# Optimization experiments

Hardware: AMD Instinct MI355X
Metric: run time of the kernel (lower is better)

Reference implementation:

```python
import jax, jax.numpy as jnp
import numpy as np

B, L, S = 1, 2048, 2048
D_MODEL, H = 1024, 16
DK = D_MODEL // H  # d_keys = d_values = 64


def sparsemax(z):
    # sparsemax along last axis: proj of z onto the simplex
    K = z.shape[-1]
    z_sorted = jnp.flip(jnp.sort(z, axis=-1), axis=-1)
    cs = jnp.cumsum(z_sorted, axis=-1)
    r = jnp.arange(1, K + 1, dtype=z.dtype)
    support = 1.0 + r * z_sorted > cs
    k = jnp.sum(support, axis=-1, keepdims=True)
    tau = (jnp.take_along_axis(cs, k.astype(jnp.int32) - 1, axis=-1) - 1.0) / k.astype(z.dtype)
    return jnp.maximum(z - tau, 0.0)


def setup_inputs() -> dict:
    key = jax.random.key(0)
    ks = jax.random.split(key, 12)
    sc = 1.0 / np.sqrt(D_MODEL)
    return {
        "queries": jax.random.normal(ks[0], (B, L, D_MODEL), jnp.float32),
        "keys": jax.random.normal(ks[1], (B, S, D_MODEL), jnp.float32),
        "values": jax.random.normal(ks[2], (B, S, D_MODEL), jnp.float32),
        "Wq": jax.random.normal(ks[3], (D_MODEL, H * DK), jnp.float32) * sc,
        "bq": jnp.zeros((H * DK,), jnp.float32),
        "Wk": jax.random.normal(ks[4], (D_MODEL, H * DK), jnp.float32) * sc,
        "bk": jnp.zeros((H * DK,), jnp.float32),
        "Wv": jax.random.normal(ks[5], (H * DK, H * DK), jnp.float32) * sc,
        "bv": jnp.zeros((H * DK,), jnp.float32),
        "Wo": jax.random.normal(ks[6], (H * DK, D_MODEL), jnp.float32) * sc,
        "bo": jnp.zeros((D_MODEL,), jnp.float32),
    }


def reference(queries, keys, values, Wq, bq, Wk, bk, Wv, bv, Wo, bo):
    # projections (note: input `values` is unused, matching the torch source)
    q = (queries @ Wq + bq).reshape(B, L, H, DK)
    k_flat = keys @ Wk + bk                      # [B,S,H*DK]
    k = k_flat.reshape(B, S, H, DK)
    v = (k_flat @ Wv + bv).reshape(B, S, H, DK)  # value_projection(key_projection(keys))
    scale = 1.0 / np.sqrt(DK)
    scores = jnp.einsum('blhe,bshe->bhls', q, k) * scale  # [B,H,L,S]
    A = sparsemax(scores)
    out = jnp.einsum('bhls,bshd->blhd', A, v)             # [B,L,H,DK]
    # mix=True: transpose(2,1) -> [B,H,L,D] then view(B,L,-1)
    out = jnp.swapaxes(out, 1, 2).reshape(B, L, H * DK)
    return out @ Wo + bo
```

## Files before the change

### kernel.cpp

```cpp
#include <hip/hip_runtime.h>
#include <hip/hip_bf16.h>


typedef __attribute__((ext_vector_type(8))) short short8;
typedef __attribute__((ext_vector_type(4))) float floatx4;

#define SRC_BF16 0
#define SRC_F32  1
#define SRC_RT   2
#define CAP 256

__device__ __forceinline__ short f2bf(float f) {
    __hip_bfloat16 h = __float2bfloat16(f);
    return *reinterpret_cast<const short*>(&h);
}
__device__ __forceinline__ unsigned short f2bfu(float f) {
    __hip_bfloat16 h = __float2bfloat16(f);
    return *reinterpret_cast<const unsigned short*>(&h);
}
__device__ __forceinline__ float bf2f(unsigned short u) {
    return __uint_as_float(((unsigned)u) << 16);
}
__device__ __forceinline__ unsigned fmap(float f) {
    unsigned u = __float_as_uint(f);
    return (u & 0x80000000u) ? ~u : (u | 0x80000000u);
}
__device__ __forceinline__ float funmap(unsigned u) {
    return (u & 0x80000000u) ? __uint_as_float(u ^ 0x80000000u) : __uint_as_float(~u);
}

__global__ void detect_k(const short* __restrict__ q, int n, int* __restrict__ flag)
{
    const int tid = threadIdx.x;
    int bad = 0;
    for (int i = tid; i < n; i += 64) {
        float f = bf2f((unsigned short)q[i]);
        if (!(fabsf(f) < 1e10f)) bad = 1;
    }
    unsigned long long m = __ballot(bad != 0);
    if (tid == 0) *flag = (m != 0ULL) ? 1 : 0;
}

__global__ __launch_bounds__(256)
void convert2_k(const void* __restrict__ s0, const void* __restrict__ s1,
                short* __restrict__ d0, short* __restrict__ d1,
                const int* __restrict__ dflag)
{
    const void* s = blockIdx.z ? s1 : s0;
    short* d = blockIdx.z ? d1 : d0;
    const size_t i = ((size_t)blockIdx.x * 256 + threadIdx.x) * 8;
    short8 o;
    if (*dflag) {
        const float4 f0 = ((const float4*)((const float*)s + i))[0];
        const float4 f1 = ((const float4*)((const float*)s + i))[1];
        o[0] = f2bf(f0.x); o[1] = f2bf(f0.y); o[2] = f2bf(f0.z); o[3] = f2bf(f0.w);
        o[4] = f2bf(f1.x); o[5] = f2bf(f1.y); o[6] = f2bf(f1.z); o[7] = f2bf(f1.w);
    } else {
        o = *(const short8*)((const short*)s + i);
    }
    *(short8*)(d + i) = o;
}

struct TP4 {
    const void* s[4];
    short* d[4];
};
__global__ __launch_bounds__(256)
void transpose4_k(TP4 p, int R, int C, const int* __restrict__ dflag)
{
    __shared__ short T[64][72];
    const int tid = threadIdx.x;
    const int bC = blockIdx.x, bR = blockIdx.y;
    const void* src = p.s[blockIdx.z];
    short* dst = p.d[blockIdx.z];
    const bool f32 = (*dflag != 0);

    const int colg = (tid & 7) * 8;
    #pragma unroll
    for (int h = 0; h < 2; ++h) {
        const int row = (tid >> 3) + 32 * h;
        const size_t idx = (size_t)(bR * 64 + row) * (size_t)C + (size_t)(bC * 64 + colg);
        short e[8];
        if (f32) {
            const float4 f0 = ((const float4*)((const float*)src + idx))[0];
            const float4 f1 = ((const float4*)((const float*)src + idx))[1];
            e[0] = f2bf(f0.x); e[1] = f2bf(f0.y); e[2] = f2bf(f0.z); e[3] = f2bf(f0.w);
            e[4] = f2bf(f1.x); e[5] = f2bf(f1.y); e[6] = f2bf(f1.z); e[7] = f2bf(f1.w);
        } else {
            short8 s = *(const short8*)((const short*)src + idx);
            #pragma unroll
            for (int j = 0; j < 8; ++j) e[j] = s[j];
        }
        #pragma unroll
        for (int j = 0; j < 8; ++j) T[colg + j][row] = e[j];
    }
    __syncthreads();
    #pragma unroll
    for (int h = 0; h < 2; ++h) {
        const int orow = (tid >> 3) + 32 * h;
        const int ocolg = (tid & 7) * 8;
        const size_t idx = (size_t)(bC * 64 + orow) * (size_t)R + (size_t)(bR * 64 + ocolg);
        *(short8*)(dst + idx) = *(const short8*)&T[orow][ocolg];
    }
}

struct GJ { const short* A; const short* B; const void* bias; void* C; };

template<int OSRC>
__global__ __launch_bounds__(256)
void gemm64_bt_k(GJ j0, GJ j1, const int* __restrict__ dflag)
{
    __shared__ __align__(16) short As[64][40];
    __shared__ __align__(16) short Bs[64][40];

    const GJ j = blockIdx.z ? j1 : j0;
    const int rtf = *dflag;

    const int tid  = threadIdx.x;
    const int bN   = blockIdx.x, bM = blockIdx.y;
    const int lane = tid & 63, wave = tid >> 6;
    const int wm   = (wave >> 1) * 32;
    const int wn   = (wave & 1) * 32;
    const int quad = lane >> 4, r16 = lane & 15;

    floatx4 acc[2][2];
    #pragma unroll
    for (int i = 0; i < 2; ++i)
        #pragma unroll
        for (int jj = 0; jj < 2; ++jj)
            acc[i][jj] = (floatx4){0.f, 0.f, 0.f, 0.f};

    const int ar = tid >> 2, ac = (tid & 3) * 8;

    for (int k0 = 0; k0 < 1024; k0 += 32) {
        *(short8*)&As[ar][ac] =
            *(const short8*)(j.A + (size_t)(bM * 64 + ar) * 1024 + (size_t)(k0 + ac));
        *(short8*)&Bs[ar][ac] =
            *(const short8*)(j.B + (size_t)(bN * 64 + ar) * 1024 + (size_t)(k0 + ac));
        __syncthreads();

        short8 a0 = *(const short8*)&As[wm + r16][quad * 8];
        short8 a1 = *(const short8*)&As[wm + 16 + r16][quad * 8];
        short8 b0 = *(const short8*)&Bs[wn + r16][quad * 8];
        short8 b1 = *(const short8*)&Bs[wn + 16 + r16][quad * 8];

        acc[0][0] = __builtin_amdgcn_mfma_f32_16x16x32_bf16(a0, b0, acc[0][0], 0, 0, 0);
        acc[0][1] = __builtin_amdgcn_mfma_f32_16x16x32_bf16(a0, b1, acc[0][1], 0, 0, 0);
        acc[1][0] = __builtin_amdgcn_mfma_f32_16x16x32_bf16(a1, b0, acc[1][0], 0, 0, 0);
        acc[1][1] = __builtin_amdgcn_mfma_f32_16x16x32_bf16(a1, b1, acc[1][1], 0, 0, 0);
        __syncthreads();
    }

    const bool of32 = (OSRC == SRC_F32) || (OSRC == SRC_RT && rtf);
    #pragma unroll
    for (int jj = 0; jj < 2; ++jj) {
        const int gc = bN * 64 + wn + jj * 16 + r16;
        const float bb = rtf ? ((const float*)j.bias)[gc]
                             : bf2f(((const unsigned short*)j.bias)[gc]);
        #pragma unroll
        for (int i = 0; i < 2; ++i) {
            #pragma unroll
            for (int rg = 0; rg < 4; ++rg) {
                const int gr = bM * 64 + wm + i * 16 + quad * 4 + rg;
                const float v = acc[i][jj][rg] + bb;
                if (of32)
                    ((float*)j.C)[(size_t)gr * 1024 + gc] = v;
                else
                    ((__hip_bfloat16*)j.C)[(size_t)gr * 1024 + gc] = __float2bfloat16(v);
            }
        }
    }
}

__global__ __launch_bounds__(256)
void attn_fused_k(const short* __restrict__ Qb, const short* __restrict__ Kb,
                  const short* __restrict__ Vb, short* __restrict__ Ob)
{
    __shared__ __align__(16) short sQ[32][72];
    __shared__ __align__(16) short sK[256][72];
    __shared__ unsigned cpk[32][CAP];
    __shared__ unsigned rmax[32];
    __shared__ int cnt[32];

    const int tid  = threadIdx.x;
    const int lane = tid & 63, wave = tid >> 6;
    const int quad = lane >> 4, r16 = lane & 15;
    const int row0 = blockIdx.x * 32;
    const int h    = blockIdx.y;
    const int sp   = (wave >> 1) * 16;
    const int hf   = wave & 1;
    const int myrow = sp + quad * 4;

    if (tid < 32) { rmax[tid] = 0u; cnt[tid] = 0; }
    {
        const int r = tid >> 3, c = (tid & 7) * 8;
        *(short8*)&sQ[r][c] = *(const short8*)(Qb + (size_t)(row0 + r) * 1024 + h * 64 + c);
    }
    __syncthreads();

    const short8 a0 = *(const short8*)&sQ[sp + r16][quad * 8];
    const short8 a1 = *(const short8*)&sQ[sp + r16][32 + quad * 8];

    for (int s0 = 0; s0 < 2048; s0 += 256) {
        #pragma unroll
        for (int i = 0; i < 8; ++i) {
            const int kr = (tid >> 3) + 32 * i, c = (tid & 7) * 8;
            *(short8*)&sK[kr][c] = *(const short8*)(Kb + (size_t)(s0 + kr) * 1024 + h * 64 + c);
        }
        __syncthreads();

        floatx4 acc[8];
        #pragma unroll
        for (int t = 0; t < 8; ++t) {
            const int ct = (hf + 2 * t) * 16;
            const short8 b0 = *(const short8*)&sK[ct + r16][quad * 8];
            const short8 b1 = *(const short8*)&sK[ct + r16][32 + quad * 8];
            floatx4 a = (floatx4){0.f, 0.f, 0.f, 0.f};
            a = __builtin_amdgcn_mfma_f32_16x16x32_bf16(a0, b0, a, 0, 0, 0);
            a = __builtin_amdgcn_mfma_f32_16x16x32_bf16(a1, b1, a, 0, 0, 0);
            #pragma unroll
            for (int rg = 0; rg < 4; ++rg) a[rg] *= 0.125f;
            acc[t] = a;
        }

        #pragma unroll
        for (int rg = 0; rg < 4; ++rg) {
            float m = acc[0][rg];
            #pragma unroll
            for (int t = 1; t < 8; ++t) m = fmaxf(m, acc[t][rg]);
            #pragma unroll
            for (int off = 1; off < 16; off <<= 1)
                m = fmaxf(m, __shfl_xor(m, off, 64));
            if (r16 == 0) atomicMax(&rmax[myrow + rg], fmap(m));
        }
        __syncthreads();

        #pragma unroll
        for (int rg = 0; rg < 4; ++rg) {
            const int row = myrow + rg;
            const float thr = funmap(rmax[row]) - 1.0f;
            #pragma unroll
            for (int t = 0; t < 8; ++t) {
                const float val = acc[t][rg];
                if (val >= thr) {
                    const int p = atomicAdd(&cnt[row], 1);
                    if (p < CAP) {
                        cpk[row][p] = ((unsigned)f2bfu(val) << 16)
                                    | (unsigned)(s0 + (hf + 2 * t) * 16 + r16);
                    }
                }
            }
        }
    }
    __syncthreads();

    const unsigned long long pre = (1ULL << lane) - 1ULL;
    for (int rr = 0; rr < 8; ++rr) {
        const int r = wave * 8 + rr;
        const int n = min(cnt[r], CAP);

        float v[4];
        unsigned short ii[4];
        #pragma unroll
        for (int i = 0; i < 4; ++i) {
            const int ix = lane + i * 64;
            if (ix < n) {
                const unsigned u = cpk[r][ix];
                v[i] = bf2f((unsigned short)(u >> 16));
                ii[i] = (unsigned short)(u & 0xFFFFu);
            } else { v[i] = -3.0e38f; ii[i] = 0; }
        }

        float tau = -3.0e38f, prevc = -1.0f;
        for (int it = 0; it < 24; ++it) {
            float s = 0.f, c = 0.f;
            #pragma unroll
            for (int i = 0; i < 4; ++i)
                if (v[i] > tau) { s += v[i]; c += 1.f; }
            #pragma unroll
            for (int off = 1; off < 64; off <<= 1) {
                s += __shfl_xor(s, off, 64);
                c += __shfl_xor(c, off, 64);
            }
            if (c == prevc) break;
            prevc = c;
            tau = (s - 1.0f) / c;
        }

        int base = 0;
        #pragma unroll
        for (int i = 0; i < 4; ++i) {
            const float p = v[i] - tau;
            const unsigned long long m = __ballot(p > 0.f);
            const int w = base + __popcll(m & pre);
            if (p > 0.f) cpk[r][w] = ((unsigned)f2bfu(p) << 16) | (unsigned)ii[i];
            base += __popcll(m);
        }
        const int msup = base;

        const unsigned short* vb = (const unsigned short*)Vb + (size_t)h * 64 + lane;
        float a0 = 0.f, a1 = 0.f, a2 = 0.f, a3 = 0.f;
        int jj = 0;
        for (; jj + 4 <= msup; jj += 4) {
            const unsigned u0 = cpk[r][jj],     u1 = cpk[r][jj + 1];
            const unsigned u2 = cpk[r][jj + 2], u3 = cpk[r][jj + 3];
            a0 += bf2f((unsigned short)(u0 >> 16)) * bf2f(vb[(size_t)(u0 & 0xFFFFu) * 1024]);
            a1 += bf2f((unsigned short)(u1 >> 16)) * bf2f(vb[(size_t)(u1 & 0xFFFFu) * 1024]);
            a2 += bf2f((unsigned short)(u2 >> 16)) * bf2f(vb[(size_t)(u2 & 0xFFFFu) * 1024]);
            a3 += bf2f((unsigned short)(u3 >> 16)) * bf2f(vb[(size_t)(u3 & 0xFFFFu) * 1024]);
        }
        for (; jj < msup; ++jj) {
            const unsigned u0 = cpk[r][jj];
            a0 += bf2f((unsigned short)(u0 >> 16)) * bf2f(vb[(size_t)(u0 & 0xFFFFu) * 1024]);
        }
        Ob[((size_t)h * 2048 + row0 + r) * 64 + lane] = f2bf(a0 + a1 + a2 + a3);
    }
}

extern "C" void kernel_launch(void* const* d_in, const int* in_sizes, int n_in,
                              void* d_out, int out_size, void* d_ws, size_t ws_size,
                              hipStream_t stream)
{
    (void)in_sizes; (void)n_in; (void)out_size; (void)ws_size;

    const void* queries = d_in[0];
    const void* keys    = d_in[1];
    const void* Wq = d_in[3];
    const void* bq = d_in[4];
    const void* Wk = d_in[5];
    const void* bk = d_in[6];
    const void* Wv = d_in[7];
    const void* bv = d_in[8];
    const void* Wo = d_in[9];
    const void* bo = d_in[10];

    const int L = 2048, DM = 1024;
    const size_t LD = (size_t)L * DM;

    int*   flag = (int*)d_ws;
    short* Qc  = (short*)((char*)d_ws + 256);
    short* Kc  = Qc + LD;
    short* WqT = Kc + LD;
    short* WkT = WqT + (size_t)DM * DM;
    short* WvT = WkT + (size_t)DM * DM;
    short* WoT = WvT + (size_t)DM * DM;
    short* Qb  = WoT + (size_t)DM * DM;
    short* Kb  = Qb + LD;
    short* Vb  = Kb + LD;
    short* Ob  = Vb + LD;

    dim3 blk(256);

    detect_k<<<dim3(1), dim3(64), 0, stream>>>((const short*)queries, 4096, flag);

    convert2_k<<<dim3((unsigned)(LD / 2048), 1, 2), blk, 0, stream>>>(
        queries, keys, Qc, Kc, flag);

    {
        TP4 p;
        p.s[0] = Wq; p.s[1] = Wk; p.s[2] = Wv; p.s[3] = Wo;
        p.d[0] = WqT; p.d[1] = WkT; p.d[2] = WvT; p.d[3] = WoT;
        transpose4_k<<<dim3(DM / 64, DM / 64, 4), blk, 0, stream>>>(p, DM, DM, flag);
    }

    {
        GJ jq{(const short*)Qc, WqT, bq, Qb};
        GJ jk{(const short*)Kc, WkT, bk, Kb};
        gemm64_bt_k<SRC_BF16><<<dim3(DM / 64, L / 64, 2), blk, 0, stream>>>(jq, jk, flag);
    }
    {
        GJ jv{(const short*)Kb, WvT, bv, Vb};
        gemm64_bt_k<SRC_BF16><<<dim3(DM / 64, L / 64, 1), blk, 0, stream>>>(jv, jv, flag);
    }

    attn_fused_k<<<dim3(L / 32, 16), blk, 0, stream>>>(Qb, Kb, Vb, Ob);

    {
        GJ jo{(const short*)Ob, WoT, bo, d_out};
        gemm64_bt_k<SRC_RT><<<dim3(DM / 64, L / 64, 1), blk, 0, stream>>>(jo, jo, flag);
    }
}
```

Measured before the change: 277.3 us.

## Tighten sparsemax candidate threshold with top-2 tracking and aggregate atomics per quad

Each thread now tracks the per-row top-two scores seen so far and uses max(g1-1, (g1+m2-1)/2) as the candidate threshold. This bound is tighter than g1-1, so fewer candidates are pushed to shared memory. Per-element atomicAdd on the row counter is replaced by one ballot-based atomicAdd per 16-lane group. The K tile shrinks to 128 rows and the candidate cap to 128, which cuts LDS use and allows a 4-blocks-per-CU launch bound for higher occupancy. The risk is that rows with more than 128 candidates are silently truncated, and there are twice as many tile iterations and syncs.

Result: faster. 271.7 us (-2.0%).

```diff
diff --git a/kernel.cpp b/kernel.cpp
--- a/kernel.cpp
+++ b/kernel.cpp
@@ -8,7 +8,7 @@
 #define SRC_BF16 0
 #define SRC_F32  1
 #define SRC_RT   2
-#define CAP 256
+#define CAP 128
 
 __device__ __forceinline__ short f2bf(float f) {
     __hip_bfloat16 h = __float2bfloat16(f);
@@ -172,12 +172,12 @@
     }
 }
 
-__global__ __launch_bounds__(256)
+__global__ __launch_bounds__(256, 4)
 void attn_fused_k(const short* __restrict__ Qb, const short* __restrict__ Kb,
                   const short* __restrict__ Vb, short* __restrict__ Ob)
 {
     __shared__ __align__(16) short sQ[32][72];
-    __shared__ __align__(16) short sK[256][72];
+    __shared__ __align__(16) short sK[128][72];
     __shared__ unsigned cpk[32][CAP];
     __shared__ unsigned rmax[32];
     __shared__ int cnt[32];
@@ -198,26 +198,30 @@
     }
     __syncthreads();
 
-    const short8 a0 = *(const short8*)&sQ[sp + r16][quad * 8];
-    const short8 a1 = *(const short8*)&sQ[sp + r16][32 + quad * 8];
-
-    for (int s0 = 0; s0 < 2048; s0 += 256) {
-        #pragma unroll
-        for (int i = 0; i < 8; ++i) {
+    const short8 qa0 = *(const short8*)&sQ[sp + r16][quad * 8];
+    const short8 qa1 = *(const short8*)&sQ[sp + r16][32 + quad * 8];
+
+    float rm1[4], rm2[4];
+    #pragma unroll
+    for (int rg = 0; rg < 4; ++rg) { rm1[rg] = -3.0e38f; rm2[rg] = -3.0e38f; }
+
+    for (int s0 = 0; s0 < 2048; s0 += 128) {
+        #pragma unroll
+        for (int i = 0; i < 4; ++i) {
             const int kr = (tid >> 3) + 32 * i, c = (tid & 7) * 8;
             *(short8*)&sK[kr][c] = *(const short8*)(Kb + (size_t)(s0 + kr) * 1024 + h * 64 + c);
         }
         __syncthreads();
 
-        floatx4 acc[8];
-        #pragma unroll
-        for (int t = 0; t < 8; ++t) {
+        floatx4 acc[4];
+        #pragma unroll
+        for (int t = 0; t < 4; ++t) {
             const int ct = (hf + 2 * t) * 16;
             const short8 b0 = *(const short8*)&sK[ct + r16][quad * 8];
             const short8 b1 = *(const short8*)&sK[ct + r16][32 + quad * 8];
             floatx4 a = (floatx4){0.f, 0.f, 0.f, 0.f};
-            a = __builtin_amdgcn_mfma_f32_16x16x32_bf16(a0, b0, a, 0, 0, 0);
-            a = __builtin_amdgcn_mfma_f32_16x16x32_bf16(a1, b1, a, 0, 0, 0);
+            a = __builtin_amdgcn_mfma_f32_16x16x32_bf16(qa0, b0, a, 0, 0, 0);
+            a = __builtin_amdgcn_mfma_f32_16x16x32_bf16(qa1, b1, a, 0, 0, 0);
             #pragma unroll
             for (int rg = 0; rg < 4; ++rg) a[rg] *= 0.125f;
             acc[t] = a;
@@ -225,29 +229,46 @@
 
         #pragma unroll
         for (int rg = 0; rg < 4; ++rg) {
-            float m = acc[0][rg];
-            #pragma unroll
-            for (int t = 1; t < 8; ++t) m = fmaxf(m, acc[t][rg]);
-            #pragma unroll
-            for (int off = 1; off < 16; off <<= 1)
-                m = fmaxf(m, __shfl_xor(m, off, 64));
-            if (r16 == 0) atomicMax(&rmax[myrow + rg], fmap(m));
+            float m1ab = fmaxf(acc[0][rg], acc[1][rg]);
+            float m2ab = fminf(acc[0][rg], acc[1][rg]);
+            float m1cd = fmaxf(acc[2][rg], acc[3][rg]);
+            float m2cd = fminf(acc[2][rg], acc[3][rg]);
+            float m1 = fmaxf(m1ab, m1cd);
+            float m2 = fmaxf(fminf(m1ab, m1cd), (m1ab >= m1cd) ? m2ab : m2cd);
+            #pragma unroll
+            for (int off = 1; off < 16; off <<= 1) {
+                const float o1 = __shfl_xor(m1, off, 64);
+                const float o2 = __shfl_xor(m2, off, 64);
+                const float n2 = fmaxf(fminf(m1, o1), (m1 >= o1) ? m2 : o2);
+                m1 = fmaxf(m1, o1);
+                m2 = n2;
+            }
+            const float n1 = fmaxf(rm1[rg], m1);
+            rm2[rg] = fmaxf(fminf(rm1[rg], m1), (rm1[rg] >= m1) ? rm2[rg] : m2);
+            rm1[rg] = n1;
+            if (r16 == 0) atomicMax(&rmax[myrow + rg], fmap(m1));
         }
         __syncthreads();
 
         #pragma unroll
         for (int rg = 0; rg < 4; ++rg) {
             const int row = myrow + rg;
-            const float thr = funmap(rmax[row]) - 1.0f;
-            #pragma unroll
-            for (int t = 0; t < 8; ++t) {
+            const float g1 = funmap(rmax[row]);
+            const float thr = fmaxf(g1 - 1.0f, 0.5f * (g1 + rm2[rg]) - 0.5f);
+            #pragma unroll
+            for (int t = 0; t < 4; ++t) {
                 const float val = acc[t][rg];
-                if (val >= thr) {
-                    const int p = atomicAdd(&cnt[row], 1);
-                    if (p < CAP) {
+                const bool keep = (val >= thr);
+                const unsigned long long m = __ballot(keep);
+                const unsigned qm = (unsigned)((m >> (quad * 16)) & 0xFFFFull);
+                int base = 0;
+                if (r16 == 0 && qm) base = atomicAdd(&cnt[row], __popc(qm));
+                base = __shfl(base, quad * 16, 64);
+                if (keep) {
+                    const int p = base + __popc(qm & ((1u << r16) - 1u));
+                    if (p < CAP)
                         cpk[row][p] = ((unsigned)f2bfu(val) << 16)
                                     | (unsigned)(s0 + (hf + 2 * t) * 16 + r16);
-                    }
                 }
             }
         }
@@ -259,10 +280,10 @@
         const int r = wave * 8 + rr;
         const int n = min(cnt[r], CAP);
 
-        float v[4];
-        unsigned short ii[4];
-        #pragma unroll
-        for (int i = 0; i < 4; ++i) {
+        float v[2];
+        unsigned short ii[2];
+        #pragma unroll
+        for (int i = 0; i < 2; ++i) {
             const int ix = lane + i * 64;
             if (ix < n) {
                 const unsigned u = cpk[r][ix];
@@ -275,7 +296,7 @@
         for (int it = 0; it < 24; ++it) {
             float s = 0.f, c = 0.f;
             #pragma unroll
-            for (int i = 0; i < 4; ++i)
+            for (int i = 0; i < 2; ++i)
                 if (v[i] > tau) { s += v[i]; c += 1.f; }
             #pragma unroll
             for (int off = 1; off < 64; off <<= 1) {
@@ -289,7 +310,7 @@
 
         int base = 0;
         #pragma unroll
-        for (int i = 0; i < 4; ++i) {
+        for (int i = 0; i < 2; ++i) {
             const float p = v[i] - tau;
             const unsigned long long m = __ballot(p > 0.f);
             const int w = base + __popcll(m & pre);
@@ -299,21 +320,21 @@
         const int msup = base;
 
         const unsigned short* vb = (const unsigned short*)Vb + (size_t)h * 64 + lane;
-        float a0 = 0.f, a1 = 0.f, a2 = 0.f, a3 = 0.f;
+        float o0 = 0.f, o1 = 0.f, o2 = 0.f, o3 = 0.f;
         int jj = 0;
         for (; jj + 4 <= msup; jj += 4) {
             const unsigned u0 = cpk[r][jj],     u1 = cpk[r][jj + 1];
             const unsigned u2 = cpk[r][jj + 2], u3 = cpk[r][jj + 3];
-            a0 += bf2f((unsigned short)(u0 >> 16)) * bf2f(vb[(size_t)(u0 & 0xFFFFu) * 1024]);
-            a1 += bf2f((unsigned short)(u1 >> 16)) * bf2f(vb[(size_t)(u1 & 0xFFFFu) * 1024]);
-            a2 += bf2f((unsigned short)(u2 >> 16)) * bf2f(vb[(size_t)(u2 & 0xFFFFu) * 1024]);
-            a3 += bf2f((unsigned short)(u3 >> 16)) * bf2f(vb[(size_t)(u3 & 0xFFFFu) * 1024]);
+            o0 += bf2f((unsigned short)(u0 >> 16)) * bf2f(vb[(size_t)(u0 & 0xFFFFu) * 1024]);
+            o1 += bf2f((unsigned short)(u1 >> 16)) * bf2f(vb[(size_t)(u1 & 0xFFFFu) * 1024]);
+            o2 += bf2f((unsigned short)(u2 >> 16)) * bf2f(vb[(size_t)(u2 & 0xFFFFu) * 1024]);
+            o3 += bf2f((unsigned short)(u3 >> 16)) * bf2f(vb[(size_t)(u3 & 0xFFFFu) * 1024]);
         }
         for (; jj < msup; ++jj) {
             const unsigned u0 = cpk[r][jj];
-            a0 += bf2f((unsigned short)(u0 >> 16)) * bf2f(vb[(size_t)(u0 & 0xFFFFu) * 1024]);
-        }
-        Ob[((size_t)h * 2048 + row0 + r) * 64 + lane] = f2bf(a0 + a1 + a2 + a3);
+            o0 += bf2f((unsigned short)(u0 >> 16)) * bf2f(vb[(size_t)(u0 & 0xFFFFu) * 1024]);
+        }
+        Ob[((size_t)h * 2048 + row0 + r) * 64 + lane] = f2bf(o0 + o1 + o2 + o3);
     }
 }
 
```
